# Kernel tuning notes

Measured on AMD Instinct MI355X. Metric: run time of the kernel, lower is better.

## Reference

```python
import math
import jax, jax.numpy as jnp
import numpy as np

BATCH = 65536
SIZE = 1024


def _even_odd_mult(p, x):
    """(1-p)*x + p*[evens..., odds...] for x of shape (B, n)."""
    B, n = x.shape
    sep = x.reshape(B, n // 2, 2).transpose(0, 2, 1).reshape(B, n)
    return (1 - p) * x + p * sep


def _reverse_mult(p1, p2, x):
    """Probabilistically reverse first half (p1) and second half (p2)."""
    B, n = x.shape
    h = n // 2
    first = x[:, :h]
    second = x[:, h:]
    first = (1 - p1) * first + p1 * first[:, ::-1]
    second = (1 - p2) * second + p2 * second[:, ::-1]
    return jnp.concatenate([first, second], axis=-1)


def setup_inputs() -> dict:
    key = jax.random.key(0)
    k1, k2 = jax.random.split(key)
    x = jax.random.normal(k1, (BATCH, SIZE), dtype=jnp.float32)
    m = int(math.log2(SIZE))
    logits = jax.random.normal(k2, (m - 1, 3), dtype=jnp.float32)
    return {"x": x, "logits": logits}


def reference(x, logits):
    size = x.shape[-1]
    m = int(math.log2(size))
    # factor i has size sizes[i]; increasing_size=True -> [4, 8, ..., size]
    sizes = [size >> i for i in range(m - 1)][::-1]
    out = x
    # forward iterates factors[::-1]: largest block size first
    for i in range(m - 2, -1, -1):
        n = sizes[i]
        prob = jax.nn.sigmoid(logits[i])
        y = out.reshape(-1, n)
        y = _even_odd_mult(prob[0], y)
        y = _reverse_mult(prob[1], prob[2], y)
        out = y.reshape(out.shape)
    return out
```

## Files before the change

### kernel.cpp

```cpp
#include <hip/hip_runtime.h>
#include <math.h>

#define TPB 64
#define ROWS 2

__device__ __forceinline__ unsigned swz(unsigned A) {
    return A ^ ((((A >> 8) ^ (A >> 11)) & 7u) << 4);
}

__device__ __forceinline__ float4 ldsrd(const char* ldsb, unsigned A) {
    return *(const float4*)(ldsb + A);
}

template<int N>
__device__ __forceinline__ void lds_stage(char* ldsb, unsigned rb, unsigned tt,
                                          float p, float p1, float p2) {
    constexpr unsigned H = N / 2;
    constexpr int L2 = (N == 512) ? 4 : (N == 256) ? 3 : 2;
    const unsigned b  = tt >> L2;
    const unsigned s  = tt & ((N / 32) - 1);
    const unsigned u0 = s * 8u;
    const unsigned bc = b * (unsigned)N;

    const unsigned Aj0  = swz(rb + 4u * (bc + u0));
    const unsigned Aj1  = swz(rb + 4u * (bc + H + u0));
    const unsigned Ajm0 = swz(rb + 4u * (bc + H - 8 - u0));
    const unsigned Ajm1 = swz(rb + 4u * (bc + N - 8 - u0));
    const unsigned Ae   = swz(rb + 4u * (bc + 2 * u0));
    const unsigned Aem  = swz(rb + 4u * (bc + 2 * H - 16 - 2 * u0));

    float j0[8], j1[8], jm0[8], jm1[8], e[16], em[16];
    *(float4*)&j0[0]  = ldsrd(ldsb, Aj0);        *(float4*)&j0[4]  = ldsrd(ldsb, Aj0 ^ 16u);
    *(float4*)&j1[0]  = ldsrd(ldsb, Aj1);        *(float4*)&j1[4]  = ldsrd(ldsb, Aj1 ^ 16u);
    *(float4*)&jm0[0] = ldsrd(ldsb, Ajm0);       *(float4*)&jm0[4] = ldsrd(ldsb, Ajm0 ^ 16u);
    *(float4*)&jm1[0] = ldsrd(ldsb, Ajm1);       *(float4*)&jm1[4] = ldsrd(ldsb, Ajm1 ^ 16u);
    *(float4*)&e[0]   = ldsrd(ldsb, Ae);         *(float4*)&e[4]   = ldsrd(ldsb, Ae ^ 16u);
    *(float4*)&e[8]   = ldsrd(ldsb, Ae ^ 32u);   *(float4*)&e[12]  = ldsrd(ldsb, Ae ^ 48u);
    *(float4*)&em[0]  = ldsrd(ldsb, Aem);        *(float4*)&em[4]  = ldsrd(ldsb, Aem ^ 16u);
    *(float4*)&em[8]  = ldsrd(ldsb, Aem ^ 32u);  *(float4*)&em[12] = ldsrd(ldsb, Aem ^ 48u);

    #pragma unroll
    for (int du = 0; du < 8; ++du) {
        {
            float yj = j0[du], yjm = jm0[7 - du];
            float yej = e[2 * du], yejm = em[14 - 2 * du];
            float a0 = fmaf(p, yej - yj, yj);
            float a1 = fmaf(p, yejm - yjm, yjm);
            float d  = a1 - a0;
            j0[du]      = fmaf(p1, d, a0);
            jm0[7 - du] = fmaf(p1, -d, a1);
        }
        {
            float zj = j1[du], zjm = jm1[7 - du];
            float zej = e[2 * du + 1], zejm = em[15 - 2 * du];
            float a0 = fmaf(p, zej - zj, zj);
            float a1 = fmaf(p, zejm - zjm, zjm);
            float d  = a1 - a0;
            j1[du]      = fmaf(p2, d, a0);
            jm1[7 - du] = fmaf(p2, -d, a1);
        }
    }
    *(float4*)(ldsb + Aj0)          = *(const float4*)&j0[0];
    *(float4*)(ldsb + (Aj0 ^ 16u))  = *(const float4*)&j0[4];
    *(float4*)(ldsb + Aj1)          = *(const float4*)&j1[0];
    *(float4*)(ldsb + (Aj1 ^ 16u))  = *(const float4*)&j1[4];
    *(float4*)(ldsb + Ajm0)         = *(const float4*)&jm0[0];
    *(float4*)(ldsb + (Ajm0 ^ 16u)) = *(const float4*)&jm0[4];
    *(float4*)(ldsb + Ajm1)         = *(const float4*)&jm1[0];
    *(float4*)(ldsb + (Ajm1 ^ 16u)) = *(const float4*)&jm1[4];
}

template<int N>
__device__ __forceinline__ void reg_stage(float* arr, float p, float p1, float p2) {
    constexpr int H = N / 2;
    float tmp[32];
    #pragma unroll
    for (int bb = 0; bb < 32; bb += N) {
        #pragma unroll
        for (int u = 0; u < N / 4; ++u) {
            {
                int j = bb + u, jm = bb + H - 1 - u;
                int ej = bb + 2 * u, ejm = bb + 2 * H - 2 - 2 * u;
                float a0 = fmaf(p, arr[ej]  - arr[j],  arr[j]);
                float a1 = fmaf(p, arr[ejm] - arr[jm], arr[jm]);
                tmp[j]  = fmaf(p1, a1 - a0, a0);
                tmp[jm] = fmaf(p1, a0 - a1, a1);
            }
            {
                int j = bb + H + u, jm = bb + 2 * H - 1 - u;
                int ej = bb + 2 * u + 1, ejm = bb + 2 * H - 1 - 2 * u;
                float a0 = fmaf(p, arr[ej]  - arr[j],  arr[j]);
                float a1 = fmaf(p, arr[ejm] - arr[jm], arr[jm]);
                tmp[j]  = fmaf(p2, a1 - a0, a0);
                tmp[jm] = fmaf(p2, a0 - a1, a1);
            }
        }
    }
    #pragma unroll
    for (int v = 0; v < 32; ++v) arr[v] = tmp[v];
}

__global__ void bpp_prep(const float* __restrict__ logits, float* __restrict__ sp) {
    int i = threadIdx.x;
    if (i < 27) sp[i] = 1.0f / (1.0f + expf(-logits[i]));
}

template<bool USE_WS>
__global__ __launch_bounds__(TPB) void bpp_main(const float* __restrict__ x,
                                                float* __restrict__ out,
                                                const float* __restrict__ spws,
                                                const float* __restrict__ logits) {
    __shared__ float lds[ROWS * 1024];
    char* ldsb = (char*)lds;
    const unsigned l = threadIdx.x;
    const size_t gbase = (size_t)blockIdx.x * (ROWS * 1024);

    float prl[27];
    if constexpr (!USE_WS) {
        #pragma unroll
        for (int i = 0; i < 27; ++i) prl[i] = 1.0f / (1.0f + expf(-logits[i]));
    }
    #define PV(i) (USE_WS ? spws[(i)] : prl[(i)])

    {
        const float4* __restrict__ gin = (const float4*)(x + gbase) + l;
        #pragma unroll
        for (int k = 0; k < 8; ++k) {
            float4 v = gin[k * 64];
            unsigned A = (unsigned)k * 1024u + l * 16u;
            *(float4*)(ldsb + swz(A)) = v;
        }
    }

    const unsigned row = l >> 5, tt = l & 31u;
    const unsigned rb = row * 4096u;

    {
        constexpr unsigned N = 1024, H = 512;
        const unsigned u0 = tt * 8u;
        const unsigned Aj0  = swz(rb + 4u * u0);
        const unsigned Aj1  = swz(rb + 4u * (H + u0));
        const unsigned Ajm0 = swz(rb + 4u * (H - 8 - u0));
        const unsigned Ajm1 = swz(rb + 4u * (N - 8 - u0));
        const unsigned Ae   = swz(rb + 4u * (2 * u0));
        const unsigned Aem  = swz(rb + 4u * (2 * H - 16 - 2 * u0));
        const float p = PV(24), p1 = PV(25), p2 = PV(26);

        float j0[8], j1[8], jm0[8], jm1[8], e[16], em[16];
        *(float4*)&j0[0]  = ldsrd(ldsb, Aj0);        *(float4*)&j0[4]  = ldsrd(ldsb, Aj0 ^ 16u);
        *(float4*)&j1[0]  = ldsrd(ldsb, Aj1);        *(float4*)&j1[4]  = ldsrd(ldsb, Aj1 ^ 16u);
        *(float4*)&jm0[0] = ldsrd(ldsb, Ajm0);       *(float4*)&jm0[4] = ldsrd(ldsb, Ajm0 ^ 16u);
        *(float4*)&jm1[0] = ldsrd(ldsb, Ajm1);       *(float4*)&jm1[4] = ldsrd(ldsb, Ajm1 ^ 16u);
        *(float4*)&e[0]   = ldsrd(ldsb, Ae);         *(float4*)&e[4]   = ldsrd(ldsb, Ae ^ 16u);
        *(float4*)&e[8]   = ldsrd(ldsb, Ae ^ 32u);   *(float4*)&e[12]  = ldsrd(ldsb, Ae ^ 48u);
        *(float4*)&em[0]  = ldsrd(ldsb, Aem);        *(float4*)&em[4]  = ldsrd(ldsb, Aem ^ 16u);
        *(float4*)&em[8]  = ldsrd(ldsb, Aem ^ 32u);  *(float4*)&em[12] = ldsrd(ldsb, Aem ^ 48u);

        #pragma unroll
        for (int du = 0; du < 8; ++du) {
            {
                float yj = j0[du], yjm = jm0[7 - du];
                float yej = e[2 * du], yejm = em[14 - 2 * du];
                float a0 = fmaf(p, yej - yj, yj);
                float a1 = fmaf(p, yejm - yjm, yjm);
                float d  = a1 - a0;
                j0[du]      = fmaf(p1, d, a0);
                jm0[7 - du] = fmaf(p1, -d, a1);
            }
            {
                float zj = j1[du], zjm = jm1[7 - du];
                float zej = e[2 * du + 1], zejm = em[15 - 2 * du];
                float a0 = fmaf(p, zej - zj, zj);
                float a1 = fmaf(p, zejm - zjm, zjm);
                float d  = a1 - a0;
                j1[du]      = fmaf(p2, d, a0);
                jm1[7 - du] = fmaf(p2, -d, a1);
            }
        }
        *(float4*)(ldsb + Aj0)          = *(const float4*)&j0[0];
        *(float4*)(ldsb + (Aj0 ^ 16u))  = *(const float4*)&j0[4];
        *(float4*)(ldsb + Aj1)          = *(const float4*)&j1[0];
        *(float4*)(ldsb + (Aj1 ^ 16u))  = *(const float4*)&j1[4];
        *(float4*)(ldsb + Ajm0)         = *(const float4*)&jm0[0];
        *(float4*)(ldsb + (Ajm0 ^ 16u)) = *(const float4*)&jm0[4];
        *(float4*)(ldsb + Ajm1)         = *(const float4*)&jm1[0];
        *(float4*)(ldsb + (Ajm1 ^ 16u)) = *(const float4*)&jm1[4];
    }
    lds_stage<512>(ldsb, rb, tt, PV(21), PV(22), PV(23));
    lds_stage<256>(ldsb, rb, tt, PV(18), PV(19), PV(20));
    lds_stage<128>(ldsb, rb, tt, PV(15), PV(16), PV(17));

    {
        const unsigned q = tt & 1u;
        const unsigned Aown = swz(rb + 128u * tt);
        const unsigned Aoth = Aown ^ 128u;
        float own[32], oth[32];
        #pragma unroll
        for (int k = 0; k < 8; ++k) {
            *(float4*)&own[4 * k] = ldsrd(ldsb, Aown ^ (16u * k));
            *(float4*)&oth[4 * k] = ldsrd(ldsb, Aoth ^ (16u * k));
        }
        const float p = PV(12);
        const float q64 = q ? PV(14) : PV(13);
        float o[32];
        #pragma unroll
        for (int u = 0; u < 16; ++u) {
            float eja = q ? oth[2 * u + 1]  : own[2 * u];
            float ejb = q ? own[31 - 2 * u] : oth[30 - 2 * u];
            float yj = own[u], yjm = own[31 - u];
            float a0 = fmaf(p, eja - yj, yj);
            float a1 = fmaf(p, ejb - yjm, yjm);
            float d  = a1 - a0;
            o[u]      = fmaf(q64, d, a0);
            o[31 - u] = fmaf(q64, -d, a1);
        }
        reg_stage<32>(o, PV(9), PV(10), PV(11));
        reg_stage<16>(o, PV(6), PV(7),  PV(8));
        reg_stage< 8>(o, PV(3), PV(4),  PV(5));
        reg_stage< 4>(o, PV(0), PV(1),  PV(2));
        #pragma unroll
        for (int k = 0; k < 8; ++k)
            *(float4*)(ldsb + (Aown ^ (16u * k))) = *(const float4*)&o[4 * k];
    }

    {
        float4* __restrict__ gout = (float4*)(out + gbase) + l;
        #pragma unroll
        for (int k = 0; k < 8; ++k) {
            unsigned A = (unsigned)k * 1024u + l * 16u;
            gout[k * 64] = *(const float4*)(ldsb + swz(A));
        }
    }
    #undef PV
}

extern "C" void kernel_launch(void* const* d_in, const int* in_sizes, int n_in,
                              void* d_out, int out_size, void* d_ws, size_t ws_size,
                              hipStream_t stream) {
    const float* x      = (const float*)d_in[0];
    const float* logits = (const float*)d_in[1];
    float* out = (float*)d_out;
    int rows = in_sizes[0] / 1024;
    int grid = rows / ROWS;
    if (ws_size >= 27 * sizeof(float)) {
        float* sp = (float*)d_ws;
        bpp_prep<<<dim3(1), dim3(32), 0, stream>>>(logits, sp);
        bpp_main<true><<<dim3(grid), dim3(TPB), 0, stream>>>(x, out, sp, logits);
    } else {
        bpp_main<false><<<dim3(grid), dim3(TPB), 0, stream>>>(x, out, nullptr, logits);
    }
}
```

Before: 124.1 us.

## Loop multiple tiles per block with register prefetch of next tile

Each block now processes several 2-row tiles in a loop, loading the next tile's input into registers while the current tile is transformed in LDS and stored. The grid shrinks accordingly, with the tile count per block chosen on the host to divide evenly. This aims to overlap global load latency with compute and cut block launch overhead, at the cost of extra registers and far fewer resident waves for latency hiding.

```diff
diff --git a/kernel.cpp b/kernel.cpp
--- a/kernel.cpp
+++ b/kernel.cpp
@@ -2,7 +2,7 @@
 #include <math.h>
 
 #define TPB 64
-#define ROWS 2
+#define NT_MAX 8
 
 __device__ __forceinline__ unsigned swz(unsigned A) {
     return A ^ ((((A >> 8) ^ (A >> 11)) & 7u) << 4);
@@ -109,11 +109,11 @@
 __global__ __launch_bounds__(TPB) void bpp_main(const float* __restrict__ x,
                                                 float* __restrict__ out,
                                                 const float* __restrict__ spws,
-                                                const float* __restrict__ logits) {
-    __shared__ float lds[ROWS * 1024];
+                                                const float* __restrict__ logits,
+                                                int nt) {
+    __shared__ float lds[2 * 1024 + 1024];
     char* ldsb = (char*)lds;
     const unsigned l = threadIdx.x;
-    const size_t gbase = (size_t)blockIdx.x * (ROWS * 1024);
 
     float prl[27];
     if constexpr (!USE_WS) {
@@ -122,113 +122,127 @@
     }
     #define PV(i) (USE_WS ? spws[(i)] : prl[(i)])
 
-    {
-        const float4* __restrict__ gin = (const float4*)(x + gbase) + l;
-        #pragma unroll
-        for (int k = 0; k < 8; ++k) {
-            float4 v = gin[k * 64];
-            unsigned A = (unsigned)k * 1024u + l * 16u;
-            *(float4*)(ldsb + swz(A)) = v;
-        }
-    }
-
     const unsigned row = l >> 5, tt = l & 31u;
     const unsigned rb = row * 4096u;
-
+    const size_t tile0 = (size_t)blockIdx.x * (unsigned)nt;
+
+    float4 pf[8];
     {
-        constexpr unsigned N = 1024, H = 512;
-        const unsigned u0 = tt * 8u;
-        const unsigned Aj0  = swz(rb + 4u * u0);
-        const unsigned Aj1  = swz(rb + 4u * (H + u0));
-        const unsigned Ajm0 = swz(rb + 4u * (H - 8 - u0));
-        const unsigned Ajm1 = swz(rb + 4u * (N - 8 - u0));
-        const unsigned Ae   = swz(rb + 4u * (2 * u0));
-        const unsigned Aem  = swz(rb + 4u * (2 * H - 16 - 2 * u0));
-        const float p = PV(24), p1 = PV(25), p2 = PV(26);
-
-        float j0[8], j1[8], jm0[8], jm1[8], e[16], em[16];
-        *(float4*)&j0[0]  = ldsrd(ldsb, Aj0);        *(float4*)&j0[4]  = ldsrd(ldsb, Aj0 ^ 16u);
-        *(float4*)&j1[0]  = ldsrd(ldsb, Aj1);        *(float4*)&j1[4]  = ldsrd(ldsb, Aj1 ^ 16u);
-        *(float4*)&jm0[0] = ldsrd(ldsb, Ajm0);       *(float4*)&jm0[4] = ldsrd(ldsb, Ajm0 ^ 16u);
-        *(float4*)&jm1[0] = ldsrd(ldsb, Ajm1);       *(float4*)&jm1[4] = ldsrd(ldsb, Ajm1 ^ 16u);
-        *(float4*)&e[0]   = ldsrd(ldsb, Ae);         *(float4*)&e[4]   = ldsrd(ldsb, Ae ^ 16u);
-        *(float4*)&e[8]   = ldsrd(ldsb, Ae ^ 32u);   *(float4*)&e[12]  = ldsrd(ldsb, Ae ^ 48u);
-        *(float4*)&em[0]  = ldsrd(ldsb, Aem);        *(float4*)&em[4]  = ldsrd(ldsb, Aem ^ 16u);
-        *(float4*)&em[8]  = ldsrd(ldsb, Aem ^ 32u);  *(float4*)&em[12] = ldsrd(ldsb, Aem ^ 48u);
-
-        #pragma unroll
-        for (int du = 0; du < 8; ++du) {
-            {
-                float yj = j0[du], yjm = jm0[7 - du];
-                float yej = e[2 * du], yejm = em[14 - 2 * du];
-                float a0 = fmaf(p, yej - yj, yj);
-                float a1 = fmaf(p, yejm - yjm, yjm);
-                float d  = a1 - a0;
-                j0[du]      = fmaf(p1, d, a0);
-                jm0[7 - du] = fmaf(p1, -d, a1);
-            }
-            {
-                float zj = j1[du], zjm = jm1[7 - du];
-                float zej = e[2 * du + 1], zejm = em[15 - 2 * du];
-                float a0 = fmaf(p, zej - zj, zj);
-                float a1 = fmaf(p, zejm - zjm, zjm);
-                float d  = a1 - a0;
-                j1[du]      = fmaf(p2, d, a0);
-                jm1[7 - du] = fmaf(p2, -d, a1);
-            }
-        }
-        *(float4*)(ldsb + Aj0)          = *(const float4*)&j0[0];
-        *(float4*)(ldsb + (Aj0 ^ 16u))  = *(const float4*)&j0[4];
-        *(float4*)(ldsb + Aj1)          = *(const float4*)&j1[0];
-        *(float4*)(ldsb + (Aj1 ^ 16u))  = *(const float4*)&j1[4];
-        *(float4*)(ldsb + Ajm0)         = *(const float4*)&jm0[0];
-        *(float4*)(ldsb + (Ajm0 ^ 16u)) = *(const float4*)&jm0[4];
-        *(float4*)(ldsb + Ajm1)         = *(const float4*)&jm1[0];
-        *(float4*)(ldsb + (Ajm1 ^ 16u)) = *(const float4*)&jm1[4];
-    }
-    lds_stage<512>(ldsb, rb, tt, PV(21), PV(22), PV(23));
-    lds_stage<256>(ldsb, rb, tt, PV(18), PV(19), PV(20));
-    lds_stage<128>(ldsb, rb, tt, PV(15), PV(16), PV(17));
-
-    {
-        const unsigned q = tt & 1u;
-        const unsigned Aown = swz(rb + 128u * tt);
-        const unsigned Aoth = Aown ^ 128u;
-        float own[32], oth[32];
-        #pragma unroll
-        for (int k = 0; k < 8; ++k) {
-            *(float4*)&own[4 * k] = ldsrd(ldsb, Aown ^ (16u * k));
-            *(float4*)&oth[4 * k] = ldsrd(ldsb, Aoth ^ (16u * k));
-        }
-        const float p = PV(12);
-        const float q64 = q ? PV(14) : PV(13);
-        float o[32];
-        #pragma unroll
-        for (int u = 0; u < 16; ++u) {
-            float eja = q ? oth[2 * u + 1]  : own[2 * u];
-            float ejb = q ? own[31 - 2 * u] : oth[30 - 2 * u];
-            float yj = own[u], yjm = own[31 - u];
-            float a0 = fmaf(p, eja - yj, yj);
-            float a1 = fmaf(p, ejb - yjm, yjm);
-            float d  = a1 - a0;
-            o[u]      = fmaf(q64, d, a0);
-            o[31 - u] = fmaf(q64, -d, a1);
-        }
-        reg_stage<32>(o, PV(9), PV(10), PV(11));
-        reg_stage<16>(o, PV(6), PV(7),  PV(8));
-        reg_stage< 8>(o, PV(3), PV(4),  PV(5));
-        reg_stage< 4>(o, PV(0), PV(1),  PV(2));
-        #pragma unroll
-        for (int k = 0; k < 8; ++k)
-            *(float4*)(ldsb + (Aown ^ (16u * k))) = *(const float4*)&o[4 * k];
-    }
-
-    {
-        float4* __restrict__ gout = (float4*)(out + gbase) + l;
+        const float4* __restrict__ gin = (const float4*)(x + tile0 * 2048u) + l;
+        #pragma unroll
+        for (int k = 0; k < 8; ++k) pf[k] = gin[k * 64];
+    }
+
+    for (int it = 0; it < nt; ++it) {
+        const size_t gofs = (tile0 + it) * 2048u;
+
         #pragma unroll
         for (int k = 0; k < 8; ++k) {
             unsigned A = (unsigned)k * 1024u + l * 16u;
-            gout[k * 64] = *(const float4*)(ldsb + swz(A));
+            *(float4*)(ldsb + swz(A)) = pf[k];
+        }
+
+        if (it + 1 < nt) {
+            const float4* __restrict__ gin = (const float4*)(x + gofs + 2048u) + l;
+            #pragma unroll
+            for (int k = 0; k < 8; ++k) pf[k] = gin[k * 64];
+        }
+
+        {
+            constexpr unsigned N = 1024, H = 512;
+            const unsigned u0 = tt * 8u;
+            const unsigned Aj0  = swz(rb + 4u * u0);
+            const unsigned Aj1  = swz(rb + 4u * (H + u0));
+            const unsigned Ajm0 = swz(rb + 4u * (H - 8 - u0));
+            const unsigned Ajm1 = swz(rb + 4u * (N - 8 - u0));
+            const unsigned Ae   = swz(rb + 4u * (2 * u0));
+            const unsigned Aem  = swz(rb + 4u * (2 * H - 16 - 2 * u0));
+            const float p = PV(24), p1 = PV(25), p2 = PV(26);
+
+            float j0[8], j1[8], jm0[8], jm1[8], e[16], em[16];
+            *(float4*)&j0[0]  = ldsrd(ldsb, Aj0);        *(float4*)&j0[4]  = ldsrd(ldsb, Aj0 ^ 16u);
+            *(float4*)&j1[0]  = ldsrd(ldsb, Aj1);        *(float4*)&j1[4]  = ldsrd(ldsb, Aj1 ^ 16u);
+            *(float4*)&jm0[0] = ldsrd(ldsb, Ajm0);       *(float4*)&jm0[4] = ldsrd(ldsb, Ajm0 ^ 16u);
+            *(float4*)&jm1[0] = ldsrd(ldsb, Ajm1);       *(float4*)&jm1[4] = ldsrd(ldsb, Ajm1 ^ 16u);
+            *(float4*)&e[0]   = ldsrd(ldsb, Ae);         *(float4*)&e[4]   = ldsrd(ldsb, Ae ^ 16u);
+            *(float4*)&e[8]   = ldsrd(ldsb, Ae ^ 32u);   *(float4*)&e[12]  = ldsrd(ldsb, Ae ^ 48u);
+            *(float4*)&em[0]  = ldsrd(ldsb, Aem);        *(float4*)&em[4]  = ldsrd(ldsb, Aem ^ 16u);
+            *(float4*)&em[8]  = ldsrd(ldsb, Aem ^ 32u);  *(float4*)&em[12] = ldsrd(ldsb, Aem ^ 48u);
+
+            #pragma unroll
+            for (int du = 0; du < 8; ++du) {
+                {
+                    float yj = j0[du], yjm = jm0[7 - du];
+                    float yej = e[2 * du], yejm = em[14 - 2 * du];
+                    float a0 = fmaf(p, yej - yj, yj);
+                    float a1 = fmaf(p, yejm - yjm, yjm);
+                    float d  = a1 - a0;
+                    j0[du]      = fmaf(p1, d, a0);
+                    jm0[7 - du] = fmaf(p1, -d, a1);
+                }
+                {
+                    float zj = j1[du], zjm = jm1[7 - du];
+                    float zej = e[2 * du + 1], zejm = em[15 - 2 * du];
+                    float a0 = fmaf(p, zej - zj, zj);
+                    float a1 = fmaf(p, zejm - zjm, zjm);
+                    float d  = a1 - a0;
+                    j1[du]      = fmaf(p2, d, a0);
+                    jm1[7 - du] = fmaf(p2, -d, a1);
+                }
+            }
+            *(float4*)(ldsb + Aj0)          = *(const float4*)&j0[0];
+            *(float4*)(ldsb + (Aj0 ^ 16u))  = *(const float4*)&j0[4];
+            *(float4*)(ldsb + Aj1)          = *(const float4*)&j1[0];
+            *(float4*)(ldsb + (Aj1 ^ 16u))  = *(const float4*)&j1[4];
+            *(float4*)(ldsb + Ajm0)         = *(const float4*)&jm0[0];
+            *(float4*)(ldsb + (Ajm0 ^ 16u)) = *(const float4*)&jm0[4];
+            *(float4*)(ldsb + Ajm1)         = *(const float4*)&jm1[0];
+            *(float4*)(ldsb + (Ajm1 ^ 16u)) = *(const float4*)&jm1[4];
+        }
+        lds_stage<512>(ldsb, rb, tt, PV(21), PV(22), PV(23));
+        lds_stage<256>(ldsb, rb, tt, PV(18), PV(19), PV(20));
+        lds_stage<128>(ldsb, rb, tt, PV(15), PV(16), PV(17));
+
+        {
+            const unsigned q = tt & 1u;
+            const unsigned Aown = swz(rb + 128u * tt);
+            const unsigned Aoth = Aown ^ 128u;
+            float own[32], oth[32];
+            #pragma unroll
+            for (int k = 0; k < 8; ++k) {
+                *(float4*)&own[4 * k] = ldsrd(ldsb, Aown ^ (16u * k));
+                *(float4*)&oth[4 * k] = ldsrd(ldsb, Aoth ^ (16u * k));
+            }
+            const float p = PV(12);
+            const float q64 = q ? PV(14) : PV(13);
+            float o[32];
+            #pragma unroll
+            for (int u = 0; u < 16; ++u) {
+                float eja = q ? oth[2 * u + 1]  : own[2 * u];
+                float ejb = q ? own[31 - 2 * u] : oth[30 - 2 * u];
+                float yj = own[u], yjm = own[31 - u];
+                float a0 = fmaf(p, eja - yj, yj);
+                float a1 = fmaf(p, ejb - yjm, yjm);
+                float d  = a1 - a0;
+                o[u]      = fmaf(q64, d, a0);
+                o[31 - u] = fmaf(q64, -d, a1);
+            }
+            reg_stage<32>(o, PV(9), PV(10), PV(11));
+            reg_stage<16>(o, PV(6), PV(7),  PV(8));
+            reg_stage< 8>(o, PV(3), PV(4),  PV(5));
+            reg_stage< 4>(o, PV(0), PV(1),  PV(2));
+            #pragma unroll
+            for (int k = 0; k < 8; ++k)
+                *(float4*)(ldsb + (Aown ^ (16u * k))) = *(const float4*)&o[4 * k];
+        }
+
+        {
+            float4* __restrict__ gout = (float4*)(out + gofs) + l;
+            #pragma unroll
+            for (int k = 0; k < 8; ++k) {
+                unsigned A = (unsigned)k * 1024u + l * 16u;
+                gout[k * 64] = *(const float4*)(ldsb + swz(A));
+            }
         }
     }
     #undef PV
@@ -240,13 +254,16 @@
     const float* x      = (const float*)d_in[0];
     const float* logits = (const float*)d_in[1];
     float* out = (float*)d_out;
-    int rows = in_sizes[0] / 1024;
-    int grid = rows / ROWS;
+    int rows  = in_sizes[0] / 1024;
+    int tiles = rows / 2;
+    int nt = NT_MAX;
+    while (nt > 1 && (tiles % nt)) nt >>= 1;
+    int grid = tiles / nt;
     if (ws_size >= 27 * sizeof(float)) {
         float* sp = (float*)d_ws;
         bpp_prep<<<dim3(1), dim3(32), 0, stream>>>(logits, sp);
-        bpp_main<true><<<dim3(grid), dim3(TPB), 0, stream>>>(x, out, sp, logits);
+        bpp_main<true><<<dim3(grid), dim3(TPB), 0, stream>>>(x, out, sp, logits, nt);
     } else {
-        bpp_main<false><<<dim3(grid), dim3(TPB), 0, stream>>>(x, out, nullptr, logits);
-    }
-}
+        bpp_main<false><<<dim3(grid), dim3(TPB), 0, stream>>>(x, out, nullptr, logits, nt);
+    }
+}
```

Result: slower. 171.0 us (+37.8%).
